# Performance work log

Measured on AMD Instinct MI355X. Metric: run time of the kernel, lower is better.

The kernel has to match this reference:

```python
import jax, jax.numpy as jnp
import numpy as np

B, C_IN, T_IN = 128, 128, 2500
C_OUT, K, STRIDE, PAD = 64, 27, 4, 13  # T_out = 625
BN_EPS = 1e-5
SURROGATE_ALPHA = 4.0


def binarize_weight(w):
    """1-bit (XNOR-Net style) weight quantization with straight-through estimator.
    w: (O, I, K). Per-output-channel scale = mean |w|."""
    alpha = jnp.mean(jnp.abs(w), axis=(1, 2), keepdims=True)
    wq = jnp.sign(w) * alpha
    return w + jax.lax.stop_gradient(wq - w)


def spike(x):
    """Heaviside spike with sigmoid surrogate gradient (STE)."""
    hard = (x > 0).astype(x.dtype)
    soft = jax.nn.sigmoid(SURROGATE_ALPHA * x)
    return soft + jax.lax.stop_gradient(hard - soft)


def setup_inputs() -> dict:
    key = jax.random.key(0)
    ks = jax.random.split(key, 8)
    scale_conv = 1.0 / np.sqrt(C_IN * K)
    scale_lin = 1.0 / np.sqrt(C_OUT)
    return {
        "x": jax.random.normal(ks[0], (B, C_IN, T_IN), dtype=jnp.float32),
        "conv_w": jax.random.normal(ks[1], (C_OUT, C_IN, K), dtype=jnp.float32) * scale_conv,
        "conv_b": jnp.zeros((C_OUT,), dtype=jnp.float32),
        "bn_gamma": jnp.ones((C_OUT,), dtype=jnp.float32),
        "bn_beta": jnp.zeros((C_OUT,), dtype=jnp.float32),
        "bn_mean": jax.random.normal(ks[2], (C_OUT,), dtype=jnp.float32) * 0.1,
        "bn_var": jax.random.uniform(ks[3], (C_OUT,), dtype=jnp.float32, minval=0.5, maxval=1.5),
        "wq": jax.random.normal(ks[4], (C_OUT, C_OUT), dtype=jnp.float32) * scale_lin,
        "wk": jax.random.normal(ks[5], (C_OUT, C_OUT), dtype=jnp.float32) * scale_lin,
        "wv": jax.random.normal(ks[6], (C_OUT, C_OUT), dtype=jnp.float32) * scale_lin,
        "wo": jax.random.normal(ks[7], (C_OUT, C_OUT), dtype=jnp.float32) * scale_lin,
    }


def reference(x, conv_w, conv_b, bn_gamma, bn_beta, bn_mean, bn_var, wq, wk, wv, wo):
    # --- 1-bit quantized conv1d, stride 4 ---
    w_bin = binarize_weight(conv_w)
    y = jax.lax.conv_general_dilated(
        x, w_bin, window_strides=(STRIDE,), padding=[(PAD, PAD)],
        dimension_numbers=("NCH", "OIH", "NCH"))
    y = y + conv_b[None, :, None]  # (B, C_OUT, 625)

    # --- BatchNorm1d (inference stats) + ELU ---
    inv = jax.lax.rsqrt(bn_var + BN_EPS)
    y = (y - bn_mean[None, :, None]) * (inv * bn_gamma)[None, :, None] + bn_beta[None, :, None]
    y = jax.nn.elu(y)

    # --- Global spiking attention (single head) ---
    s = spike(y)                                   # (B, C, T) binary spikes
    q = jnp.einsum("oc,bct->bot", wq, s)           # (B, C, T)
    k = jnp.einsum("oc,bct->bot", wk, s)
    v = jnp.einsum("oc,bct->bot", wv, y)
    scores = jnp.einsum("bct,bcs->bts", q, k) / jnp.sqrt(jnp.asarray(C_OUT, y.dtype))
    attn = jax.nn.softmax(scores, axis=-1)         # (B, T, T)
    ctx = jnp.einsum("bts,bcs->bct", attn, v)      # (B, C, T)
    out = y + jnp.einsum("oc,bct->bot", wo, ctx)   # residual
    return out
```

## Files before the change

### kernel.cpp

```cpp
#include <hip/hip_runtime.h>
#include <math.h>

#define B_    128
#define CIN   128
#define TIN   2500
#define COUT  64
#define KW    27
#define TOUT  625
#define TPAD  640
#define CTT   32
#define GROWS 152

typedef __bf16 bf16x8 __attribute__((ext_vector_type(8)));
typedef float  f32x4  __attribute__((ext_vector_type(4)));

__device__ __forceinline__ unsigned short f32_to_bf16_rne(float v) {
    unsigned u = __float_as_uint(v);
    u += 0x7FFFu + ((u >> 16) & 1u);
    return (unsigned short)(u >> 16);
}

__device__ __forceinline__ f32x4 mfma_bf16(bf16x8 a, bf16x8 b, f32x4 c) {
    return __builtin_amdgcn_mfma_f32_16x16x32_bf16(a, b, c, 0, 0, 0);
}

__global__ void binarize_kernel(const float* __restrict__ w,
                                unsigned* __restrict__ sgn2,
                                float* __restrict__ alpha_out) {
    int o = blockIdx.x, tid = threadIdx.x;
    __shared__ float red[256];
    const float* wo_ = w + (size_t)o * (CIN * KW);
    float s = 0.f;
    for (int idx = tid; idx < CIN * KW; idx += 256) s += fabsf(wo_[idx]);
    red[tid] = s;
    __syncthreads();
    for (int st = 128; st > 0; st >>= 1) {
        if (tid < st) red[tid] += red[tid + st];
        __syncthreads();
    }
    if (tid == 0) alpha_out[o] = red[0] / (float)(CIN * KW);

    for (int t = tid; t < KW * 4; t += 256) {
        int kk = t >> 2, kg = t & 3;
        unsigned u = 0;
#pragma unroll
        for (int cs = 0; cs < 4; cs++) {
#pragma unroll
            for (int j = 0; j < 8; j++) {
                int c = cs * 32 + kg * 8 + j;
                float v = wo_[c * KW + kk];
                unsigned bit = (v > 0.f) ? 0u : 1u;
                u |= bit << (cs * 8 + j);
            }
        }
        sgn2[(kk * 4 + kg) * 64 + o] = u;
    }
}

__global__ void transpose_w_kernel(const float* __restrict__ wq, const float* __restrict__ wk,
                                   const float* __restrict__ wv, const float* __restrict__ wo,
                                   const float* __restrict__ conv_b, const float* __restrict__ gamma_,
                                   const float* __restrict__ beta_, const float* __restrict__ mean_,
                                   const float* __restrict__ var_, const float* __restrict__ alpha_,
                                   unsigned short* __restrict__ w3_h, unsigned short* __restrict__ w3_l,
                                   unsigned short* __restrict__ wo_h, unsigned short* __restrict__ wo_l,
                                   float* __restrict__ scA, float* __restrict__ scB) {
    if (blockIdx.x < 3) {
        const float* srcs[3] = {wq, wk, wv};
        const float* src = srcs[blockIdx.x];
        unsigned short* dh = w3_h + (size_t)blockIdx.x * 4096;
        unsigned short* dl = w3_l + (size_t)blockIdx.x * 4096;
        for (int idx = threadIdx.x; idx < 4096; idx += 256) {
            float v = src[idx];
            unsigned short h = f32_to_bf16_rne(v);
            float hf = __uint_as_float((unsigned)h << 16);
            dh[idx] = h;
            dl[idx] = f32_to_bf16_rne(v - hf);
        }
    } else if (blockIdx.x == 3) {
        for (int idx = threadIdx.x; idx < 4096; idx += 256) {
            float v = wo[idx];
            unsigned short h = f32_to_bf16_rne(v);
            float hf = __uint_as_float((unsigned)h << 16);
            wo_h[idx] = h;
            wo_l[idx] = f32_to_bf16_rne(v - hf);
        }
    } else {
        int o = threadIdx.x;
        if (o < 64) {
            float inv = rsqrtf(var_[o] + 1e-5f);
            float G = gamma_[o] * inv;
            scA[o] = alpha_[o] * G;
            scB[o] = (conv_b[o] - mean_[o]) * G + beta_[o];
        }
    }
}

__global__ __launch_bounds__(256, 4) void conv_kernel(
    const float* __restrict__ x, const unsigned* __restrict__ sgn2,
    const float* __restrict__ scA, const float* __restrict__ scB,
    const unsigned short* __restrict__ w3_h, const unsigned short* __restrict__ w3_l,
    float* __restrict__ y_out,
    unsigned short* __restrict__ q_h, unsigned short* __restrict__ k_h,
    unsigned short* __restrict__ vT_h)
{
    __shared__ __align__(16) unsigned short xhi[GROWS * 128];
    __shared__ __align__(16) unsigned long long sgnlut[16];
    unsigned short* y_sh = xhi;
    unsigned short* s_sh = xhi + 2048;
    unsigned short* q_sh = xhi + 4096;
    unsigned short* k_sh = xhi + 6144;
    unsigned short* v_sh = xhi + 8192;

    int b = blockIdx.y;
    int t0 = blockIdx.x * CTT;
    int tid = threadIdx.x;

    if (tid < 16) {
        unsigned long long e = 0;
#pragma unroll
        for (int j = 0; j < 4; ++j) {
            unsigned long long h = ((tid >> j) & 1) ? 0xBF80ull : 0x3F80ull;
            e |= h << (16 * j);
        }
        sgnlut[tid] = e;
    }

    const float* xb = x + (size_t)b * CIN * TIN;
    int gbase = 4 * t0 - 13;
    for (int task = tid; task < 16 * GROWS; task += 256) {
        int c8 = task / GROWS, gl = task - c8 * GROWS;
        int g = gbase + gl;
        bool valid = (gl < 151) && ((unsigned)g < (unsigned)TIN);
        float vs[8];
#pragma unroll
        for (int j = 0; j < 8; j++)
            vs[j] = valid ? xb[(size_t)(c8 * 8 + j) * TIN + g] : 0.f;
        union { unsigned u[4]; uint4 q; } H;
#pragma unroll
        for (int j = 0; j < 4; j++) {
            unsigned short h0 = f32_to_bf16_rne(vs[2 * j]);
            unsigned short h1 = f32_to_bf16_rne(vs[2 * j + 1]);
            H.u[j] = (unsigned)h0 | ((unsigned)h1 << 16);
        }
        int c8p = c8 ^ ((gl >> 2) & 15);
        *(uint4*)(xhi + gl * 128 + c8p * 8) = H.q;
    }
    __syncthreads();

    int wave = tid >> 6, lane = tid & 63;
    int o0 = wave * 16;
    int n = lane & 15, kg = lane >> 4;

    f32x4 acc0 = {0.f, 0.f, 0.f, 0.f};
    f32x4 acc1 = {0.f, 0.f, 0.f, 0.f};

    const unsigned* sgb = sgn2 + (size_t)kg * 64 + o0 + n;
    unsigned sa = sgb[0];

#pragma unroll 1
    for (int kk = 0; kk < KW; ++kk) {
        unsigned na = 0;
        if (kk < KW - 1) na = sgb[(kk + 1) * 256];
        int gl = 4 * n + kk;
        int rot = (gl >> 2) & 15;
        const unsigned short* xr0 = xhi + gl * 128;
        const unsigned short* xr1 = xr0 + 8192;
#pragma unroll
        for (int cs = 0; cs < 4; ++cs) {
            int c8p = (cs * 4 + kg) ^ rot;
            bf16x8 b0 = *(const bf16x8*)(xr0 + c8p * 8);
            bf16x8 b1 = *(const bf16x8*)(xr1 + c8p * 8);
            unsigned byte = (sa >> (8 * cs)) & 0xFFu;
            union { unsigned long long u[2]; bf16x8 v; } A;
            A.u[0] = sgnlut[byte & 15u];
            A.u[1] = sgnlut[byte >> 4];
            acc0 = mfma_bf16(A.v, b0, acc0);
            acc1 = mfma_bf16(A.v, b1, acc1);
        }
        sa = na;
    }

    int quad = kg, col = n;
    unsigned long long ypk[2], spk[2];
#pragma unroll
    for (int tt = 0; tt < 2; ++tt) {
        int t_g = t0 + tt * 16 + col;
        f32x4 a = tt ? acc1 : acc0;
        unsigned long long yp = 0, sp = 0;
#pragma unroll
        for (int r = 0; r < 4; ++r) {
            int o = o0 + quad * 4 + r;
            float s = a[r] * scA[o] + scB[o];
            float yv = s > 0.f ? s : expm1f(s);
            if (t_g < TOUT) {
                y_out[((size_t)b * COUT + o) * TOUT + t_g] = yv;
                yp |= (unsigned long long)f32_to_bf16_rne(yv) << (16 * r);
                if (yv > 0.f) sp |= 0x3F80ull << (16 * r);
            }
        }
        ypk[tt] = yp; spk[tt] = sp;
    }
    __syncthreads();

    int c8w = (o0 >> 3) + (quad >> 1);
    int cof = (quad & 1) * 4;
#pragma unroll
    for (int tt = 0; tt < 2; ++tt) {
        int tl = tt * 16 + col;
        int idx = tl * 64 + ((c8w ^ (tl & 7)) << 3) + cof;
        *(unsigned long long*)(y_sh + idx) = ypk[tt];
        *(unsigned long long*)(s_sh + idx) = spk[tt];
    }
    __syncthreads();

    bf16x8 sf[2][2], yf[2][2];
#pragma unroll
    for (int tt = 0; tt < 2; ++tt)
#pragma unroll
        for (int ks = 0; ks < 2; ++ks) {
            int tl = tt * 16 + col;
            int idx = tl * 64 + (((ks * 4 + quad) ^ (tl & 7)) << 3);
            sf[tt][ks] = *(const bf16x8*)(s_sh + idx);
            yf[tt][ks] = *(const bf16x8*)(y_sh + idx);
        }
    size_t wofs = (size_t)(o0 + col) * 64 + quad * 8;
    f32x4 qa[2], ka[2], va[2];
#pragma unroll
    for (int tt = 0; tt < 2; ++tt) {
        qa[tt] = (f32x4){0.f, 0.f, 0.f, 0.f};
        ka[tt] = (f32x4){0.f, 0.f, 0.f, 0.f};
        va[tt] = (f32x4){0.f, 0.f, 0.f, 0.f};
    }
#pragma unroll
    for (int ks = 0; ks < 2; ++ks) {
        bf16x8 aqh = *(const bf16x8*)(w3_h + wofs + ks * 32);
        bf16x8 aql = *(const bf16x8*)(w3_l + wofs + ks * 32);
        bf16x8 akh = *(const bf16x8*)(w3_h + 4096 + wofs + ks * 32);
        bf16x8 akl = *(const bf16x8*)(w3_l + 4096 + wofs + ks * 32);
        bf16x8 avh = *(const bf16x8*)(w3_h + 8192 + wofs + ks * 32);
        bf16x8 avl = *(const bf16x8*)(w3_l + 8192 + wofs + ks * 32);
#pragma unroll
        for (int tt = 0; tt < 2; ++tt) {
            qa[tt] = mfma_bf16(aqh, sf[tt][ks], qa[tt]);
            qa[tt] = mfma_bf16(aql, sf[tt][ks], qa[tt]);
            ka[tt] = mfma_bf16(akh, sf[tt][ks], ka[tt]);
            ka[tt] = mfma_bf16(akl, sf[tt][ks], ka[tt]);
            va[tt] = mfma_bf16(avh, yf[tt][ks], va[tt]);
            va[tt] = mfma_bf16(avl, yf[tt][ks], va[tt]);
        }
    }
#pragma unroll
    for (int tt = 0; tt < 2; ++tt) {
        int tl = tt * 16 + col;
        int idx = tl * 64 + ((c8w ^ (tl & 7)) << 3) + cof;
        unsigned long long qp = 0, kp = 0;
#pragma unroll
        for (int r = 0; r < 4; ++r) {
            qp |= (unsigned long long)f32_to_bf16_rne(qa[tt][r]) << (16 * r);
            kp |= (unsigned long long)f32_to_bf16_rne(ka[tt][r]) << (16 * r);
        }
        *(unsigned long long*)(q_sh + idx) = qp;
        *(unsigned long long*)(k_sh + idx) = kp;
#pragma unroll
        for (int r = 0; r < 4; ++r) {
            int c = o0 + quad * 4 + r;
            int vidx = c * 32 + (((tt * 2 + (col >> 3)) ^ quad) << 3) + (col & 7);
            v_sh[vidx] = f32_to_bf16_rne(va[tt][r]);
        }
    }
    __syncthreads();

    {
        int tl = tid >> 3, seg = tid & 7;
        int idx = tl * 64 + ((seg ^ (tl & 7)) << 3);
        uint4 qv = *(const uint4*)(q_sh + idx);
        uint4 kv = *(const uint4*)(k_sh + idx);
        size_t go = ((size_t)b * TPAD + t0 + tl) * 64 + seg * 8;
        *(uint4*)(q_h + go) = qv;
        *(uint4*)(k_h + go) = kv;
        int c = tid >> 2, ts = tid & 3;
        int vidx = c * 32 + ((ts ^ ((c >> 2) & 3)) << 3);
        uint4 vv = *(const uint4*)(v_sh + vidx);
        *(uint4*)(vT_h + ((size_t)b * 64 + c) * TPAD + t0 + ts * 8) = vv;
    }
}

__global__ __launch_bounds__(512, 3) void attn_kernel(
    const unsigned short* __restrict__ q_h, const unsigned short* __restrict__ k_h,
    const unsigned short* __restrict__ vT_h, const float* __restrict__ y,
    const unsigned short* __restrict__ wo_h, const unsigned short* __restrict__ wo_l,
    float* __restrict__ out)
{
    __shared__ __align__(16) float sc_sh[16 * 648];
    __shared__ float ctx_sh[2 * 64 * 17];
    __shared__ float rden[16];

    int b = blockIdx.y, t0 = blockIdx.x * 16, tid = threadIdx.x;
    int wave = tid >> 6, lane = tid & 63;
    int quad = lane >> 4, nlo = lane & 15;

    const unsigned short* qb = q_h + ((size_t)b * TPAD + t0 + nlo) * 64 + quad * 8;
    bf16x8 qa0 = *(const bf16x8*)(qb);
    bf16x8 qa1 = *(const bf16x8*)(qb + 32);
    const unsigned short* kbase = k_h + (size_t)b * TPAD * 64 + quad * 8;
#pragma unroll 5
    for (int nt = 0; nt < 5; ++nt) {
        int s = wave * 80 + nt * 16 + nlo;
        const unsigned short* krow = kbase + (size_t)s * 64;
        bf16x8 kb0 = *(const bf16x8*)(krow);
        bf16x8 kb1 = *(const bf16x8*)(krow + 32);
        f32x4 acc = {0.f, 0.f, 0.f, 0.f};
        acc = mfma_bf16(qa0, kb0, acc);
        acc = mfma_bf16(qa1, kb1, acc);
#pragma unroll
        for (int r = 0; r < 4; ++r)
            sc_sh[(quad * 4 + r) * 648 + s] = acc[r] * 0.125f;
    }
    __syncthreads();

    int ti1 = tid >> 5, sg = tid & 31;
    float* srow = &sc_sh[ti1 * 648];
    float mx = -3.0e38f;
    for (int s = sg; s < TOUT; s += 32) mx = fmaxf(mx, srow[s]);
#pragma unroll
    for (int off = 16; off >= 1; off >>= 1) mx = fmaxf(mx, __shfl_xor(mx, off));

    unsigned short* prow = (unsigned short*)srow;
    float sum = 0.f;
#pragma unroll
    for (int k2 = 0; k2 < 10; ++k2) {
        int s = 2 * sg + 64 * k2;
        float2 v2 = *(const float2*)(srow + s);
        float e0 = (s     < TOUT) ? __expf(v2.x - mx) : 0.f;
        float e1 = (s + 1 < TOUT) ? __expf(v2.y - mx) : 0.f;
        sum += e0 + e1;
        unsigned u0 = __float_as_uint(e0); u0 += 0x7FFFu + ((u0 >> 16) & 1u);
        unsigned u1 = __float_as_uint(e1); u1 += 0x7FFFu + ((u1 >> 16) & 1u);
        *(unsigned*)(prow + s) = (u0 >> 16) | (u1 & 0xFFFF0000u);
    }
#pragma unroll
    for (int off = 16; off >= 1; off >>= 1) sum += __shfl_xor(sum, off);
    if (sg == 0) rden[ti1] = 1.f / sum;
    __syncthreads();

    int cw = (wave & 3) * 16, kh = wave >> 2;
    const unsigned short* vb = vT_h + ((size_t)b * 64 + cw + nlo) * TPAD;
    const unsigned short* pb = (const unsigned short*)sc_sh + nlo * 1296;
    f32x4 cacc = {0.f, 0.f, 0.f, 0.f};
    int ks0 = kh * 10;
#pragma unroll 5
    for (int i = 0; i < 10; ++i) {
        int ks = ks0 + i;
        bf16x8 pv = *(const bf16x8*)(pb + ks * 32 + quad * 8);
        bf16x8 v8 = *(const bf16x8*)(vb + ks * 32 + quad * 8);
        cacc = mfma_bf16(pv, v8, cacc);
    }
#pragma unroll
    for (int r = 0; r < 4; ++r)
        ctx_sh[kh * 1088 + (cw + nlo) * 17 + quad * 4 + r] = cacc[r] * rden[quad * 4 + r];
    __syncthreads();

    if (wave < 4) {
        const unsigned short* woh = wo_h + (size_t)(wave * 16 + nlo) * 64 + quad * 8;
        const unsigned short* wol = wo_l + (size_t)(wave * 16 + nlo) * 64 + quad * 8;
        f32x4 oacc = {0.f, 0.f, 0.f, 0.f};
#pragma unroll
        for (int ks = 0; ks < 2; ++ks) {
            union { unsigned short u[8]; bf16x8 v; } Bc;
#pragma unroll
            for (int j = 0; j < 8; ++j) {
                int c = ks * 32 + quad * 8 + j;
                float cv = ctx_sh[c * 17 + nlo] + ctx_sh[1088 + c * 17 + nlo];
                Bc.u[j] = f32_to_bf16_rne(cv);
            }
            bf16x8 ah = *(const bf16x8*)(woh + ks * 32);
            bf16x8 al = *(const bf16x8*)(wol + ks * 32);
            oacc = mfma_bf16(ah, Bc.v, oacc);
            oacc = mfma_bf16(al, Bc.v, oacc);
        }
        int t_g = t0 + nlo;
        if (t_g < TOUT) {
#pragma unroll
            for (int r = 0; r < 4; ++r) {
                int o = wave * 16 + quad * 4 + r;
                size_t off = ((size_t)b * COUT + o) * TOUT + t_g;
                out[off] = y[off] + oacc[r];
            }
        }
    }
}

extern "C" void kernel_launch(void* const* d_in, const int* in_sizes, int n_in,
                              void* d_out, int out_size, void* d_ws, size_t ws_size,
                              hipStream_t stream) {
    const float* x        = (const float*)d_in[0];
    const float* conv_w   = (const float*)d_in[1];
    const float* conv_b   = (const float*)d_in[2];
    const float* bn_gamma = (const float*)d_in[3];
    const float* bn_beta  = (const float*)d_in[4];
    const float* bn_mean  = (const float*)d_in[5];
    const float* bn_var   = (const float*)d_in[6];
    const float* wq       = (const float*)d_in[7];
    const float* wk       = (const float*)d_in[8];
    const float* wv       = (const float*)d_in[9];
    const float* wo       = (const float*)d_in[10];
    float* out = (float*)d_out;
    float* ws  = (float*)d_ws;

    unsigned* sgn2        = (unsigned*)ws;
    float* alpha          = ws + 110592;
    float* scA            = ws + 110656;
    float* scB            = ws + 110720;
    unsigned short* w3_h  = (unsigned short*)(ws + 110848);
    unsigned short* w3_l  = (unsigned short*)(ws + 116992);
    unsigned short* wo_h  = (unsigned short*)(ws + 123136);
    unsigned short* wo_l  = (unsigned short*)(ws + 125184);
    float* yb             = ws + 131072;
    unsigned short* q_h   = (unsigned short*)(ws + 5251072);
    unsigned short* k_h   = (unsigned short*)(ws + 7872512);
    unsigned short* vT_h  = (unsigned short*)(ws + 10493952);

    hipLaunchKernelGGL(binarize_kernel, dim3(64), dim3(256), 0, stream, conv_w, sgn2, alpha);
    hipLaunchKernelGGL(transpose_w_kernel, dim3(5), dim3(256), 0, stream,
                       wq, wk, wv, wo, conv_b, bn_gamma, bn_beta, bn_mean, bn_var, alpha,
                       w3_h, w3_l, wo_h, wo_l, scA, scB);
    hipLaunchKernelGGL(conv_kernel, dim3(20, 128), dim3(256), 0, stream,
                       x, sgn2, scA, scB, w3_h, w3_l, yb, q_h, k_h, vT_h);
    hipLaunchKernelGGL(attn_kernel, dim3(40, 128), dim3(512), 0, stream,
                       q_h, k_h, vT_h, yb, wo_h, wo_l, out);
}
```

Measured before the change: 433.0 us.

## Halve conv tile width and remap block IDs for XCD-aware locality

Conv blocks now cover 16 output timesteps instead of 32. This roughly halves shared memory and register use per block, doubles the grid, and raises the launch-bounds occupancy target. Both conv and attention kernels also remap linear block IDs so that the 8 interleaved dispatch groups (likely XCDs) each get contiguous batch/time ranges, which should improve L2 reuse. The cost is more redundant halo loads of x, since 87 input rows are now staged per 16 outputs versus 151 per 32, plus more blocks overall.

```diff
diff --git a/kernel.cpp b/kernel.cpp
--- a/kernel.cpp
+++ b/kernel.cpp
@@ -8,8 +8,8 @@
 #define KW    27
 #define TOUT  625
 #define TPAD  640
-#define CTT   32
-#define GROWS 152
+#define CTT   16
+#define GR2   88
 
 typedef __bf16 bf16x8 __attribute__((ext_vector_type(8)));
 typedef float  f32x4  __attribute__((ext_vector_type(4)));
@@ -96,7 +96,7 @@
     }
 }
 
-__global__ __launch_bounds__(256, 4) void conv_kernel(
+__global__ __launch_bounds__(256, 7) void conv_kernel(
     const float* __restrict__ x, const unsigned* __restrict__ sgn2,
     const float* __restrict__ scA, const float* __restrict__ scB,
     const unsigned short* __restrict__ w3_h, const unsigned short* __restrict__ w3_l,
@@ -104,17 +104,19 @@
     unsigned short* __restrict__ q_h, unsigned short* __restrict__ k_h,
     unsigned short* __restrict__ vT_h)
 {
-    __shared__ __align__(16) unsigned short xhi[GROWS * 128];
+    __shared__ __align__(16) unsigned short xhi[GR2 * 128];
     __shared__ __align__(16) unsigned long long sgnlut[16];
     unsigned short* y_sh = xhi;
-    unsigned short* s_sh = xhi + 2048;
-    unsigned short* q_sh = xhi + 4096;
-    unsigned short* k_sh = xhi + 6144;
-    unsigned short* v_sh = xhi + 8192;
-
-    int b = blockIdx.y;
-    int t0 = blockIdx.x * CTT;
+    unsigned short* s_sh = xhi + 1024;
+    unsigned short* q_sh = xhi + 2048;
+    unsigned short* k_sh = xhi + 3072;
+    unsigned short* v_sh = xhi + 4096;
+
     int tid = threadIdx.x;
+    int id = blockIdx.x + 40 * blockIdx.y;
+    int nid = (id & 7) * 640 + (id >> 3);
+    int b = nid / 40;
+    int t0 = (nid - b * 40) * CTT;
 
     if (tid < 16) {
         unsigned long long e = 0;
@@ -128,10 +130,10 @@
 
     const float* xb = x + (size_t)b * CIN * TIN;
     int gbase = 4 * t0 - 13;
-    for (int task = tid; task < 16 * GROWS; task += 256) {
-        int c8 = task / GROWS, gl = task - c8 * GROWS;
+    for (int task = tid; task < 16 * GR2; task += 256) {
+        int c8 = task / GR2, gl = task - c8 * GR2;
         int g = gbase + gl;
-        bool valid = (gl < 151) && ((unsigned)g < (unsigned)TIN);
+        bool valid = (gl < 87) && ((unsigned)g < (unsigned)TIN);
         float vs[8];
 #pragma unroll
         for (int j = 0; j < 8; j++)
@@ -152,9 +154,7 @@
     int o0 = wave * 16;
     int n = lane & 15, kg = lane >> 4;
 
-    f32x4 acc0 = {0.f, 0.f, 0.f, 0.f};
-    f32x4 acc1 = {0.f, 0.f, 0.f, 0.f};
-
+    f32x4 acc = {0.f, 0.f, 0.f, 0.f};
     const unsigned* sgb = sgn2 + (size_t)kg * 64 + o0 + n;
     unsigned sa = sgb[0];
 
@@ -165,73 +165,53 @@
         int gl = 4 * n + kk;
         int rot = (gl >> 2) & 15;
         const unsigned short* xr0 = xhi + gl * 128;
-        const unsigned short* xr1 = xr0 + 8192;
 #pragma unroll
         for (int cs = 0; cs < 4; ++cs) {
             int c8p = (cs * 4 + kg) ^ rot;
             bf16x8 b0 = *(const bf16x8*)(xr0 + c8p * 8);
-            bf16x8 b1 = *(const bf16x8*)(xr1 + c8p * 8);
             unsigned byte = (sa >> (8 * cs)) & 0xFFu;
             union { unsigned long long u[2]; bf16x8 v; } A;
             A.u[0] = sgnlut[byte & 15u];
             A.u[1] = sgnlut[byte >> 4];
-            acc0 = mfma_bf16(A.v, b0, acc0);
-            acc1 = mfma_bf16(A.v, b1, acc1);
+            acc = mfma_bf16(A.v, b0, acc);
         }
         sa = na;
     }
 
     int quad = kg, col = n;
-    unsigned long long ypk[2], spk[2];
-#pragma unroll
-    for (int tt = 0; tt < 2; ++tt) {
-        int t_g = t0 + tt * 16 + col;
-        f32x4 a = tt ? acc1 : acc0;
-        unsigned long long yp = 0, sp = 0;
-#pragma unroll
-        for (int r = 0; r < 4; ++r) {
-            int o = o0 + quad * 4 + r;
-            float s = a[r] * scA[o] + scB[o];
-            float yv = s > 0.f ? s : expm1f(s);
-            if (t_g < TOUT) {
-                y_out[((size_t)b * COUT + o) * TOUT + t_g] = yv;
-                yp |= (unsigned long long)f32_to_bf16_rne(yv) << (16 * r);
-                if (yv > 0.f) sp |= 0x3F80ull << (16 * r);
-            }
-        }
-        ypk[tt] = yp; spk[tt] = sp;
+    int t_g = t0 + col;
+    unsigned long long ypk = 0, spk = 0;
+#pragma unroll
+    for (int r = 0; r < 4; ++r) {
+        int o = o0 + quad * 4 + r;
+        float s = acc[r] * scA[o] + scB[o];
+        float yv = s > 0.f ? s : expm1f(s);
+        if (t_g < TOUT) {
+            y_out[((size_t)b * COUT + o) * TOUT + t_g] = yv;
+            ypk |= (unsigned long long)f32_to_bf16_rne(yv) << (16 * r);
+            if (yv > 0.f) spk |= 0x3F80ull << (16 * r);
+        }
     }
     __syncthreads();
 
     int c8w = (o0 >> 3) + (quad >> 1);
     int cof = (quad & 1) * 4;
-#pragma unroll
-    for (int tt = 0; tt < 2; ++tt) {
-        int tl = tt * 16 + col;
-        int idx = tl * 64 + ((c8w ^ (tl & 7)) << 3) + cof;
-        *(unsigned long long*)(y_sh + idx) = ypk[tt];
-        *(unsigned long long*)(s_sh + idx) = spk[tt];
-    }
-    __syncthreads();
-
-    bf16x8 sf[2][2], yf[2][2];
-#pragma unroll
-    for (int tt = 0; tt < 2; ++tt)
-#pragma unroll
-        for (int ks = 0; ks < 2; ++ks) {
-            int tl = tt * 16 + col;
-            int idx = tl * 64 + (((ks * 4 + quad) ^ (tl & 7)) << 3);
-            sf[tt][ks] = *(const bf16x8*)(s_sh + idx);
-            yf[tt][ks] = *(const bf16x8*)(y_sh + idx);
-        }
+    int idxw = col * 64 + ((c8w ^ (col & 7)) << 3) + cof;
+    *(unsigned long long*)(y_sh + idxw) = ypk;
+    *(unsigned long long*)(s_sh + idxw) = spk;
+    __syncthreads();
+
+    bf16x8 sf[2], yf[2];
+#pragma unroll
+    for (int ks = 0; ks < 2; ++ks) {
+        int idx = col * 64 + (((ks * 4 + quad) ^ (col & 7)) << 3);
+        sf[ks] = *(const bf16x8*)(s_sh + idx);
+        yf[ks] = *(const bf16x8*)(y_sh + idx);
+    }
     size_t wofs = (size_t)(o0 + col) * 64 + quad * 8;
-    f32x4 qa[2], ka[2], va[2];
-#pragma unroll
-    for (int tt = 0; tt < 2; ++tt) {
-        qa[tt] = (f32x4){0.f, 0.f, 0.f, 0.f};
-        ka[tt] = (f32x4){0.f, 0.f, 0.f, 0.f};
-        va[tt] = (f32x4){0.f, 0.f, 0.f, 0.f};
-    }
+    f32x4 qa = {0.f, 0.f, 0.f, 0.f};
+    f32x4 ka = {0.f, 0.f, 0.f, 0.f};
+    f32x4 va = {0.f, 0.f, 0.f, 0.f};
 #pragma unroll
     for (int ks = 0; ks < 2; ++ks) {
         bf16x8 aqh = *(const bf16x8*)(w3_h + wofs + ks * 32);
@@ -240,49 +220,43 @@
         bf16x8 akl = *(const bf16x8*)(w3_l + 4096 + wofs + ks * 32);
         bf16x8 avh = *(const bf16x8*)(w3_h + 8192 + wofs + ks * 32);
         bf16x8 avl = *(const bf16x8*)(w3_l + 8192 + wofs + ks * 32);
-#pragma unroll
-        for (int tt = 0; tt < 2; ++tt) {
-            qa[tt] = mfma_bf16(aqh, sf[tt][ks], qa[tt]);
-            qa[tt] = mfma_bf16(aql, sf[tt][ks], qa[tt]);
-            ka[tt] = mfma_bf16(akh, sf[tt][ks], ka[tt]);
-            ka[tt] = mfma_bf16(akl, sf[tt][ks], ka[tt]);
-            va[tt] = mfma_bf16(avh, yf[tt][ks], va[tt]);
-            va[tt] = mfma_bf16(avl, yf[tt][ks], va[tt]);
-        }
-    }
-#pragma unroll
-    for (int tt = 0; tt < 2; ++tt) {
-        int tl = tt * 16 + col;
-        int idx = tl * 64 + ((c8w ^ (tl & 7)) << 3) + cof;
+        qa = mfma_bf16(aqh, sf[ks], qa);
+        qa = mfma_bf16(aql, sf[ks], qa);
+        ka = mfma_bf16(akh, sf[ks], ka);
+        ka = mfma_bf16(akl, sf[ks], ka);
+        va = mfma_bf16(avh, yf[ks], va);
+        va = mfma_bf16(avl, yf[ks], va);
+    }
+    {
         unsigned long long qp = 0, kp = 0;
 #pragma unroll
         for (int r = 0; r < 4; ++r) {
-            qp |= (unsigned long long)f32_to_bf16_rne(qa[tt][r]) << (16 * r);
-            kp |= (unsigned long long)f32_to_bf16_rne(ka[tt][r]) << (16 * r);
-        }
-        *(unsigned long long*)(q_sh + idx) = qp;
-        *(unsigned long long*)(k_sh + idx) = kp;
+            qp |= (unsigned long long)f32_to_bf16_rne(qa[r]) << (16 * r);
+            kp |= (unsigned long long)f32_to_bf16_rne(ka[r]) << (16 * r);
+        }
+        *(unsigned long long*)(q_sh + idxw) = qp;
+        *(unsigned long long*)(k_sh + idxw) = kp;
 #pragma unroll
         for (int r = 0; r < 4; ++r) {
             int c = o0 + quad * 4 + r;
-            int vidx = c * 32 + (((tt * 2 + (col >> 3)) ^ quad) << 3) + (col & 7);
-            v_sh[vidx] = f32_to_bf16_rne(va[tt][r]);
+            v_sh[c * 16 + col] = f32_to_bf16_rne(va[r]);
         }
     }
     __syncthreads();
 
     {
-        int tl = tid >> 3, seg = tid & 7;
+        int task = tid & 127;
+        int tl = task >> 3, seg = task & 7;
         int idx = tl * 64 + ((seg ^ (tl & 7)) << 3);
-        uint4 qv = *(const uint4*)(q_sh + idx);
-        uint4 kv = *(const uint4*)(k_sh + idx);
-        size_t go = ((size_t)b * TPAD + t0 + tl) * 64 + seg * 8;
-        *(uint4*)(q_h + go) = qv;
-        *(uint4*)(k_h + go) = kv;
-        int c = tid >> 2, ts = tid & 3;
-        int vidx = c * 32 + ((ts ^ ((c >> 2) & 3)) << 3);
-        uint4 vv = *(const uint4*)(v_sh + vidx);
-        *(uint4*)(vT_h + ((size_t)b * 64 + c) * TPAD + t0 + ts * 8) = vv;
+        const unsigned short* srcp = (tid < 128) ? q_sh : k_sh;
+        unsigned short* dstp = (tid < 128) ? q_h : k_h;
+        uint4 val = *(const uint4*)(srcp + idx);
+        *(uint4*)(dstp + ((size_t)b * TPAD + t0 + tl) * 64 + seg * 8) = val;
+        if (tid < 128) {
+            int c = tid >> 1, ts = tid & 1;
+            uint4 vv = *(const uint4*)(v_sh + c * 16 + ts * 8);
+            *(uint4*)(vT_h + ((size_t)b * 64 + c) * TPAD + t0 + ts * 8) = vv;
+        }
     }
 }
 
@@ -296,7 +270,12 @@
     __shared__ float ctx_sh[2 * 64 * 17];
     __shared__ float rden[16];
 
-    int b = blockIdx.y, t0 = blockIdx.x * 16, tid = threadIdx.x;
+    int tid = threadIdx.x;
+    int id = blockIdx.x + 40 * blockIdx.y;
+    int nid = (id & 7) * 640 + (id >> 3);
+    int b = nid / 40;
+    int t0 = (nid - b * 40) * 16;
+
     int wave = tid >> 6, lane = tid & 63;
     int quad = lane >> 4, nlo = lane & 15;
 
@@ -425,7 +404,7 @@
     hipLaunchKernelGGL(transpose_w_kernel, dim3(5), dim3(256), 0, stream,
                        wq, wk, wv, wo, conv_b, bn_gamma, bn_beta, bn_mean, bn_var, alpha,
                        w3_h, w3_l, wo_h, wo_l, scA, scB);
-    hipLaunchKernelGGL(conv_kernel, dim3(20, 128), dim3(256), 0, stream,
+    hipLaunchKernelGGL(conv_kernel, dim3(40, 128), dim3(256), 0, stream,
                        x, sgn2, scA, scB, w3_h, w3_l, yb, q_h, k_h, vT_h);
     hipLaunchKernelGGL(attn_kernel, dim3(40, 128), dim3(512), 0, stream,
                        q_h, k_h, vT_h, yb, wo_h, wo_l, out);
```

New measurement: 438.6 us. No clear change (+1.3%).
